# Kernel optimization log

Measured on AMD Instinct MI355X. Metric: run time of the kernel, lower is better.

The kernel has to match this reference:

```python
import jax, jax.numpy as jnp
import numpy as np

HIDDEN = 128
INPUT_SIZE = 64
NUM_ACTIONS = 16
BATCH = 65536


def _uniform(key, shape, scale):
    return jax.random.uniform(key, shape, jnp.float32, -scale, scale)


def setup_inputs() -> dict:
    key = jax.random.key(0)
    ks = jax.random.split(key, 14)
    s = 1.0 / np.sqrt(HIDDEN)  # pytorch LSTM/Linear init scale
    return {
        "x": jax.random.normal(ks[0], (BATCH, INPUT_SIZE), jnp.float32),
        # layer 0 LSTM weights (gate order: i, f, g, o)
        "Wih0": _uniform(ks[1], (4 * HIDDEN, INPUT_SIZE), s),
        "Whh0": _uniform(ks[2], (4 * HIDDEN, HIDDEN), s),
        "bih0": _uniform(ks[3], (4 * HIDDEN,), s),
        "bhh0": _uniform(ks[4], (4 * HIDDEN,), s),
        # layer 1 LSTM weights
        "Wih1": _uniform(ks[5], (4 * HIDDEN, HIDDEN), s),
        "Whh1": _uniform(ks[6], (4 * HIDDEN, HIDDEN), s),
        "bih1": _uniform(ks[7], (4 * HIDDEN,), s),
        "bhh1": _uniform(ks[8], (4 * HIDDEN,), s),
        # policy / value heads
        "Wp": _uniform(ks[9], (NUM_ACTIONS, HIDDEN), s),
        "bp": _uniform(ks[10], (NUM_ACTIONS,), s),
        "Wv": _uniform(ks[11], (1, HIDDEN), s),
        "bv": _uniform(ks[12], (1,), s),
    }


def _lstm_cell(x, h, c, Wih, Whh, bih, bhh):
    # gates: [B, 4H], pytorch gate order i, f, g, o
    g = x @ Wih.T + bih + h @ Whh.T + bhh
    i, f, gg, o = jnp.split(g, 4, axis=-1)
    i = jax.nn.sigmoid(i)
    f = jax.nn.sigmoid(f)
    gg = jnp.tanh(gg)
    o = jax.nn.sigmoid(o)
    c2 = f * c + i * gg
    h2 = o * jnp.tanh(c2)
    return h2, c2


def reference(x, Wih0, Whh0, bih0, bhh0, Wih1, Whh1, bih1, bhh1, Wp, bp, Wv, bv):
    B = x.shape[0]
    z = jnp.zeros((B, HIDDEN), x.dtype)  # state=None -> zero init
    # seq_len == 1: single step through the 2-layer stack
    h0, c0 = _lstm_cell(x, z, z, Wih0, Whh0, bih0, bhh0)
    h1, c1 = _lstm_cell(h0, z, z, Wih1, Whh1, bih1, bhh1)
    out = h1[None]  # [1, B, H] like pytorch LSTM output
    policy = out @ Wp.T + bp  # gumbel=True -> raw logits
    value = out @ Wv.T + bv
    return policy, value
```

## Files before the change

kernel.cpp:

```cpp
#include <hip/hip_runtime.h>
#include <hip/hip_bf16.h>

#define BATCH 65536
#define IN    64
#define H     128
#define NA    16
#define NBLK  256
#define TPB   512

#define NW0   3072
#define NW1   6144
#define NPH   512
#define OW1   3072
#define OPH   9216
#define OBIAS 9728
#define NTOT  9920

typedef __bf16 bf16x8 __attribute__((ext_vector_type(8)));
typedef float  f32x4  __attribute__((ext_vector_type(4)));

union Frag { uint4 u; bf16x8 v; };
struct F32x8 { float4 a, b; };

#define EXP2F(v) __builtin_amdgcn_exp2f(v)
#define RCPF(v)  __builtin_amdgcn_rcpf(v)
#define K1 1.442695041f
#define K2 2.885390082f

__device__ __forceinline__ F32x8 ld8f(const float* p) {
    F32x8 r;
    r.a = *reinterpret_cast<const float4*>(p);
    r.b = *reinterpret_cast<const float4*>(p + 4);
    return r;
}
__device__ __forceinline__ Frag cvt8(F32x8 x) {
    Frag f;
    f.v[0]=(__bf16)x.a.x; f.v[1]=(__bf16)x.a.y; f.v[2]=(__bf16)x.a.z; f.v[3]=(__bf16)x.a.w;
    f.v[4]=(__bf16)x.b.x; f.v[5]=(__bf16)x.b.y; f.v[6]=(__bf16)x.b.z; f.v[7]=(__bf16)x.b.w;
    return f;
}
__device__ __forceinline__ Frag cvt44(float4 a, float4 b) {
    Frag f;
    f.v[0]=(__bf16)a.x; f.v[1]=(__bf16)a.y; f.v[2]=(__bf16)a.z; f.v[3]=(__bf16)a.w;
    f.v[4]=(__bf16)b.x; f.v[5]=(__bf16)b.y; f.v[6]=(__bf16)b.z; f.v[7]=(__bf16)b.w;
    return f;
}
__device__ __forceinline__ unsigned pk2(float lo, float hi) {
    unsigned short l = __builtin_bit_cast(unsigned short, (__bf16)lo);
    unsigned short h = __builtin_bit_cast(unsigned short, (__bf16)hi);
    return (unsigned)l | ((unsigned)h << 16);
}
__device__ __forceinline__ float clamp30(float v) {
    return __builtin_fminf(__builtin_fmaxf(v, -30.0f), 30.0f);
}
__device__ __forceinline__ float lstm_h(float ip, float gp, float op) {
    ip = clamp30(ip); gp = clamp30(gp); op = clamp30(op);
    const float Ei = EXP2F(-K1 * ip);
    const float Eg = EXP2F( K2 * gp);
    const float c2 = (Eg - 1.0f) * RCPF((1.0f + Ei) * (Eg + 1.0f));
    const float Eo = EXP2F(-K1 * op);
    const float Ec = EXP2F( K2 * c2);
    return (Ec - 1.0f) * RCPF((1.0f + Eo) * (Ec + 1.0f));
}

__device__ __forceinline__ int igo_row(int j) {
    const int g = j >> 7, h = j & 127;
    return h + ((g == 0) ? 0 : (g + 1) * 128);
}

__global__ __launch_bounds__(256)
void lstm_prep(const float* __restrict__ Wih0,
               const float* __restrict__ bih0,
               const float* __restrict__ bhh0,
               const float* __restrict__ Wih1,
               const float* __restrict__ bih1,
               const float* __restrict__ bhh1,
               const float* __restrict__ Wp,
               const float* __restrict__ Wv,
               uint4* __restrict__ ws)
{
    const int G = blockIdx.x * 256 + threadIdx.x;
    if (G < NW0) {
        const int j = G >> 3, s = G & 7;
        const int srow = igo_row(j);
        Frag f = cvt8(ld8f(Wih0 + (size_t)srow * IN + s * 8));
        ws[(j << 3) + (s ^ (j & 7))] = f.u;
    } else if (G < OPH) {
        const int t = G - OW1;
        const int j = t >> 4, s = t & 15;
        const int srow = igo_row(j);
        const int kt = s >> 2, qq = s & 3;
        const float* pA = Wih1 + (size_t)srow * H + kt * 32 + qq * 4;
        Frag f = cvt44(*reinterpret_cast<const float4*>(pA),
                       *reinterpret_cast<const float4*>(pA + 16));
        ws[OW1 + (j << 4) + (s ^ (j & 7))] = f.u;
    } else if (G < OBIAS) {
        const int t = G - OPH;
        const int j = t >> 4, s = t & 15;
        const int kt = s >> 2, qq = s & 3;
        Frag f;
        if (j <= 16) {
            const float* base = (j < 16) ? (Wp + (size_t)j * H) : Wv;
            const float* pA = base + kt * 32 + qq * 4;
            f = cvt44(*reinterpret_cast<const float4*>(pA),
                      *reinterpret_cast<const float4*>(pA + 16));
        } else {
            f.u = make_uint4(0u, 0u, 0u, 0u);
        }
        ws[OPH + (j << 4) + (s ^ (j & 7))] = f.u;
    } else if (G < NTOT) {
        const int fbase = (G - OBIAS) * 4;
        float4 r;
#pragma unroll
        for (int e = 0; e < 4; ++e) {
            const int i = fbase + e;
            float v;
            if (i < 384) { const int sr = igo_row(i);        v = bih0[sr] + bhh0[sr]; }
            else         { const int sr = igo_row(i - 384);  v = bih1[sr] + bhh1[sr]; }
            reinterpret_cast<float*>(&r)[e] = v;
        }
        ws[G] = __builtin_bit_cast(uint4, r);
    }
}

__global__ __launch_bounds__(TPB, 2)
void lstm_fused(const float* __restrict__ x,
                const uint4* __restrict__ ws,
                const float* __restrict__ bp,
                const float* __restrict__ bv,
                float* __restrict__ out)
{
    __shared__ __align__(16) uint4 smem[NTOT];

    const int tid  = threadIdx.x;
    const int wave = tid >> 6;
    const int lane = tid & 63;
    const int q    = lane >> 4;
    const int m    = lane & 15;
    const int rbase = blockIdx.x * 256 + wave * 32;
    const f32x4 vzero = {0.f, 0.f, 0.f, 0.f};

    F32x8 xr[2][2];
#pragma unroll
    for (int s2 = 0; s2 < 2; ++s2) {
        const float* xp = x + (size_t)(rbase + s2 * 16 + m) * IN + q * 8;
        xr[s2][0] = ld8f(xp);
        xr[s2][1] = ld8f(xp + 32);
    }
    const float4 bpr = *reinterpret_cast<const float4*>(bp + q * 4);
    const float  bvv = bv[0];

#pragma unroll
    for (int i = tid; i < NTOT; i += TPB) smem[i] = ws[i];

    __syncthreads();

    const uint4* w0s = smem;
    const uint4* w1s = smem + OW1;
    const uint4* wph = smem + OPH;
    const float* b0s = reinterpret_cast<const float*>(smem + OBIAS);
    const float* b1s = b0s + 384;

    const int swz = m & 7;
    Frag xb[2][2];
#pragma unroll
    for (int s2 = 0; s2 < 2; ++s2) {
        xb[s2][0] = cvt8(xr[s2][0]);
        xb[s2][1] = cvt8(xr[s2][1]);
    }

    unsigned hw0[2][16];
#pragma unroll
    for (int nc = 0; nc < 8; ++nc) {
        f32x4 acc[3][2];
#pragma unroll
        for (int g = 0; g < 3; ++g) { acc[g][0] = vzero; acc[g][1] = vzero; }
#pragma unroll
        for (int g = 0; g < 3; ++g) {
            const int n = g * 128 + nc * 16 + m;
#pragma unroll
            for (int kt = 0; kt < 2; ++kt) {
                Frag a; a.u = w0s[(n << 3) + ((kt * 4 + q) ^ swz)];
#pragma unroll
                for (int s2 = 0; s2 < 2; ++s2)
                    acc[g][s2] = __builtin_amdgcn_mfma_f32_16x16x32_bf16(
                        a.v, xb[s2][kt].v, acc[g][s2], 0, 0, 0);
            }
        }
        const f32x4 bI = *reinterpret_cast<const f32x4*>(b0s +       nc * 16 + q * 4);
        const f32x4 bG = *reinterpret_cast<const f32x4*>(b0s + 128 + nc * 16 + q * 4);
        const f32x4 bO = *reinterpret_cast<const f32x4*>(b0s + 256 + nc * 16 + q * 4);
#pragma unroll
        for (int s2 = 0; s2 < 2; ++s2)
#pragma unroll
            for (int u = 0; u < 2; ++u) {
                const float ha = lstm_h(acc[0][s2][2*u]   + bI[2*u],
                                        acc[1][s2][2*u]   + bG[2*u],
                                        acc[2][s2][2*u]   + bO[2*u]);
                const float hb = lstm_h(acc[0][s2][2*u+1] + bI[2*u+1],
                                        acc[1][s2][2*u+1] + bG[2*u+1],
                                        acc[2][s2][2*u+1] + bO[2*u+1]);
                hw0[s2][nc * 2 + u] = pk2(ha, hb);
            }
    }

    unsigned hw1[2][16];
#pragma unroll
    for (int nc = 0; nc < 8; ++nc) {
        f32x4 acc[3][2];
#pragma unroll
        for (int g = 0; g < 3; ++g) { acc[g][0] = vzero; acc[g][1] = vzero; }
#pragma unroll
        for (int kt = 0; kt < 4; ++kt) {
            Frag b[2];
#pragma unroll
            for (int s2 = 0; s2 < 2; ++s2)
                b[s2].u = make_uint4(hw0[s2][4*kt], hw0[s2][4*kt+1],
                                     hw0[s2][4*kt+2], hw0[s2][4*kt+3]);
#pragma unroll
            for (int g = 0; g < 3; ++g) {
                const int n = g * 128 + nc * 16 + m;
                Frag a; a.u = w1s[(n << 4) + ((kt * 4 + q) ^ swz)];
#pragma unroll
                for (int s2 = 0; s2 < 2; ++s2)
                    acc[g][s2] = __builtin_amdgcn_mfma_f32_16x16x32_bf16(
                        a.v, b[s2].v, acc[g][s2], 0, 0, 0);
            }
        }
        const f32x4 bI = *reinterpret_cast<const f32x4*>(b1s +       nc * 16 + q * 4);
        const f32x4 bG = *reinterpret_cast<const f32x4*>(b1s + 128 + nc * 16 + q * 4);
        const f32x4 bO = *reinterpret_cast<const f32x4*>(b1s + 256 + nc * 16 + q * 4);
#pragma unroll
        for (int s2 = 0; s2 < 2; ++s2)
#pragma unroll
            for (int u = 0; u < 2; ++u) {
                const float ha = lstm_h(acc[0][s2][2*u]   + bI[2*u],
                                        acc[1][s2][2*u]   + bG[2*u],
                                        acc[2][s2][2*u]   + bO[2*u]);
                const float hb = lstm_h(acc[0][s2][2*u+1] + bI[2*u+1],
                                        acc[1][s2][2*u+1] + bG[2*u+1],
                                        acc[2][s2][2*u+1] + bO[2*u+1]);
                hw1[s2][nc * 2 + u] = pk2(ha, hb);
            }
    }

    f32x4 ap[2], av[2];
    ap[0] = vzero; ap[1] = vzero; av[0] = vzero; av[1] = vzero;
#pragma unroll
    for (int kt = 0; kt < 4; ++kt) {
        Frag a0; a0.u = wph[( m       << 4) + ((kt * 4 + q) ^ swz)];
        Frag a1; a1.u = wph[((16 + m) << 4) + ((kt * 4 + q) ^ swz)];
#pragma unroll
        for (int s2 = 0; s2 < 2; ++s2) {
            Frag b; b.u = make_uint4(hw1[s2][4*kt], hw1[s2][4*kt+1],
                                     hw1[s2][4*kt+2], hw1[s2][4*kt+3]);
            ap[s2] = __builtin_amdgcn_mfma_f32_16x16x32_bf16(a0.v, b.v, ap[s2], 0, 0, 0);
            av[s2] = __builtin_amdgcn_mfma_f32_16x16x32_bf16(a1.v, b.v, av[s2], 0, 0, 0);
        }
    }
#pragma unroll
    for (int s2 = 0; s2 < 2; ++s2) {
        const int row = rbase + s2 * 16 + m;
        f32x4 po;
        po[0] = ap[s2][0] + bpr.x; po[1] = ap[s2][1] + bpr.y;
        po[2] = ap[s2][2] + bpr.z; po[3] = ap[s2][3] + bpr.w;
        *reinterpret_cast<f32x4*>(out + (size_t)row * NA + q * 4) = po;
        if (q == 0) out[(size_t)BATCH * NA + row] = av[s2][0] + bvv;
    }
}

extern "C" void kernel_launch(void* const* d_in, const int* in_sizes, int n_in,
                              void* d_out, int out_size, void* d_ws, size_t ws_size,
                              hipStream_t stream) {
    uint4* ws = (uint4*)d_ws;
    lstm_prep<<<dim3((NTOT + 255) / 256), dim3(256), 0, stream>>>(
        (const float*)d_in[1], (const float*)d_in[3], (const float*)d_in[4],
        (const float*)d_in[5], (const float*)d_in[7], (const float*)d_in[8],
        (const float*)d_in[9], (const float*)d_in[11], ws);
    lstm_fused<<<dim3(NBLK), dim3(TPB), 0, stream>>>(
        (const float*)d_in[0], ws,
        (const float*)d_in[10], (const float*)d_in[12], (float*)d_out);
}
```

Before: 110.4 us.

## Drop LDS weight staging, read weights from global, widen per-wave batch tile

The fused kernel no longer copies the packed weights into shared memory behind a block barrier. It reads the MFMA A-fragments straight from the global workspace, relying on L1/L2 caching, so the prep kernel's XOR swizzle is removed. Each wave now handles 64 rows instead of 32, with 256 threads per block, so every weight fragment load feeds twice as many MFMAs. Biases are folded into the accumulator initialisation, the clamping is removed, and the gate math is written over float pairs. The risks are global load latency in the inner loop, higher register pressure from four row tiles, and possible overflow in exp2 without the clamp.

```diff
diff --git a/kernel.cpp b/kernel.cpp
--- a/kernel.cpp
+++ b/kernel.cpp
@@ -6,11 +6,8 @@
 #define H     128
 #define NA    16
 #define NBLK  256
-#define TPB   512
-
-#define NW0   3072
-#define NW1   6144
-#define NPH   512
+#define TPB   256
+
 #define OW1   3072
 #define OPH   9216
 #define OBIAS 9728
@@ -18,6 +15,7 @@
 
 typedef __bf16 bf16x8 __attribute__((ext_vector_type(8)));
 typedef float  f32x4  __attribute__((ext_vector_type(4)));
+typedef float  f32x2  __attribute__((ext_vector_type(2)));
 
 union Frag { uint4 u; bf16x8 v; };
 struct F32x8 { float4 a, b; };
@@ -50,17 +48,23 @@
     unsigned short h = __builtin_bit_cast(unsigned short, (__bf16)hi);
     return (unsigned)l | ((unsigned)h << 16);
 }
-__device__ __forceinline__ float clamp30(float v) {
-    return __builtin_fminf(__builtin_fmaxf(v, -30.0f), 30.0f);
-}
-__device__ __forceinline__ float lstm_h(float ip, float gp, float op) {
-    ip = clamp30(ip); gp = clamp30(gp); op = clamp30(op);
-    const float Ei = EXP2F(-K1 * ip);
-    const float Eg = EXP2F( K2 * gp);
-    const float c2 = (Eg - 1.0f) * RCPF((1.0f + Ei) * (Eg + 1.0f));
-    const float Eo = EXP2F(-K1 * op);
-    const float Ec = EXP2F( K2 * c2);
-    return (Ec - 1.0f) * RCPF((1.0f + Eo) * (Ec + 1.0f));
+
+__device__ __forceinline__ unsigned lstm_h2(f32x2 ip, f32x2 gp, f32x2 op) {
+    const f32x2 ai = ip * (-K1);
+    const f32x2 ag = gp * ( K2);
+    f32x2 Ei; Ei[0]=EXP2F(ai[0]); Ei[1]=EXP2F(ai[1]);
+    f32x2 Eg; Eg[0]=EXP2F(ag[0]); Eg[1]=EXP2F(ag[1]);
+    const f32x2 dn = (Ei + 1.0f) * (Eg + 1.0f);
+    f32x2 rd; rd[0]=RCPF(dn[0]); rd[1]=RCPF(dn[1]);
+    const f32x2 c2 = (Eg - 1.0f) * rd;
+    const f32x2 ao = op * (-K1);
+    const f32x2 ac = c2 * ( K2);
+    f32x2 Eo; Eo[0]=EXP2F(ao[0]); Eo[1]=EXP2F(ao[1]);
+    f32x2 Ec; Ec[0]=EXP2F(ac[0]); Ec[1]=EXP2F(ac[1]);
+    const f32x2 dh = (Eo + 1.0f) * (Ec + 1.0f);
+    f32x2 rh; rh[0]=RCPF(dh[0]); rh[1]=RCPF(dh[1]);
+    const f32x2 h = (Ec - 1.0f) * rh;
+    return pk2(h[0], h[1]);
 }
 
 __device__ __forceinline__ int igo_row(int j) {
@@ -80,11 +84,11 @@
                uint4* __restrict__ ws)
 {
     const int G = blockIdx.x * 256 + threadIdx.x;
-    if (G < NW0) {
+    if (G < OW1) {
         const int j = G >> 3, s = G & 7;
         const int srow = igo_row(j);
         Frag f = cvt8(ld8f(Wih0 + (size_t)srow * IN + s * 8));
-        ws[(j << 3) + (s ^ (j & 7))] = f.u;
+        ws[(j << 3) + s] = f.u;
     } else if (G < OPH) {
         const int t = G - OW1;
         const int j = t >> 4, s = t & 15;
@@ -93,7 +97,7 @@
         const float* pA = Wih1 + (size_t)srow * H + kt * 32 + qq * 4;
         Frag f = cvt44(*reinterpret_cast<const float4*>(pA),
                        *reinterpret_cast<const float4*>(pA + 16));
-        ws[OW1 + (j << 4) + (s ^ (j & 7))] = f.u;
+        ws[OW1 + (j << 4) + s] = f.u;
     } else if (G < OBIAS) {
         const int t = G - OPH;
         const int j = t >> 4, s = t & 15;
@@ -107,7 +111,7 @@
         } else {
             f.u = make_uint4(0u, 0u, 0u, 0u);
         }
-        ws[OPH + (j << 4) + (s ^ (j & 7))] = f.u;
+        ws[OPH + (j << 4) + s] = f.u;
     } else if (G < NTOT) {
         const int fbase = (G - OBIAS) * 4;
         float4 r;
@@ -130,142 +134,128 @@
                 const float* __restrict__ bv,
                 float* __restrict__ out)
 {
-    __shared__ __align__(16) uint4 smem[NTOT];
-
     const int tid  = threadIdx.x;
     const int wave = tid >> 6;
     const int lane = tid & 63;
     const int q    = lane >> 4;
     const int m    = lane & 15;
-    const int rbase = blockIdx.x * 256 + wave * 32;
+    const int rbase = blockIdx.x * 256 + wave * 64;
     const f32x4 vzero = {0.f, 0.f, 0.f, 0.f};
 
-    F32x8 xr[2][2];
-#pragma unroll
-    for (int s2 = 0; s2 < 2; ++s2) {
-        const float* xp = x + (size_t)(rbase + s2 * 16 + m) * IN + q * 8;
-        xr[s2][0] = ld8f(xp);
-        xr[s2][1] = ld8f(xp + 32);
+    F32x8 xr[4][2];
+#pragma unroll
+    for (int s4 = 0; s4 < 4; ++s4) {
+        const float* xp = x + (size_t)(rbase + s4 * 16 + m) * IN + q * 8;
+        xr[s4][0] = ld8f(xp);
+        xr[s4][1] = ld8f(xp + 32);
     }
     const float4 bpr = *reinterpret_cast<const float4*>(bp + q * 4);
     const float  bvv = bv[0];
-
-#pragma unroll
-    for (int i = tid; i < NTOT; i += TPB) smem[i] = ws[i];
-
-    __syncthreads();
-
-    const uint4* w0s = smem;
-    const uint4* w1s = smem + OW1;
-    const uint4* wph = smem + OPH;
-    const float* b0s = reinterpret_cast<const float*>(smem + OBIAS);
-    const float* b1s = b0s + 384;
-
-    const int swz = m & 7;
-    Frag xb[2][2];
-#pragma unroll
-    for (int s2 = 0; s2 < 2; ++s2) {
-        xb[s2][0] = cvt8(xr[s2][0]);
-        xb[s2][1] = cvt8(xr[s2][1]);
-    }
-
-    unsigned hw0[2][16];
+    const float* bias = reinterpret_cast<const float*>(ws + OBIAS);
+
+    Frag xb[4][2];
+#pragma unroll
+    for (int s4 = 0; s4 < 4; ++s4) {
+        xb[s4][0] = cvt8(xr[s4][0]);
+        xb[s4][1] = cvt8(xr[s4][1]);
+    }
+
+    unsigned hw0[4][16];
 #pragma unroll
     for (int nc = 0; nc < 8; ++nc) {
-        f32x4 acc[3][2];
-#pragma unroll
-        for (int g = 0; g < 3; ++g) { acc[g][0] = vzero; acc[g][1] = vzero; }
+        const f32x4 bI = *reinterpret_cast<const f32x4*>(bias +       nc * 16 + q * 4);
+        const f32x4 bG = *reinterpret_cast<const f32x4*>(bias + 128 + nc * 16 + q * 4);
+        const f32x4 bO = *reinterpret_cast<const f32x4*>(bias + 256 + nc * 16 + q * 4);
+        f32x4 acc[3][4];
+#pragma unroll
+        for (int s4 = 0; s4 < 4; ++s4) {
+            acc[0][s4] = bI; acc[1][s4] = bG; acc[2][s4] = bO;
+        }
 #pragma unroll
         for (int g = 0; g < 3; ++g) {
             const int n = g * 128 + nc * 16 + m;
 #pragma unroll
             for (int kt = 0; kt < 2; ++kt) {
-                Frag a; a.u = w0s[(n << 3) + ((kt * 4 + q) ^ swz)];
-#pragma unroll
-                for (int s2 = 0; s2 < 2; ++s2)
-                    acc[g][s2] = __builtin_amdgcn_mfma_f32_16x16x32_bf16(
-                        a.v, xb[s2][kt].v, acc[g][s2], 0, 0, 0);
-            }
-        }
-        const f32x4 bI = *reinterpret_cast<const f32x4*>(b0s +       nc * 16 + q * 4);
-        const f32x4 bG = *reinterpret_cast<const f32x4*>(b0s + 128 + nc * 16 + q * 4);
-        const f32x4 bO = *reinterpret_cast<const f32x4*>(b0s + 256 + nc * 16 + q * 4);
-#pragma unroll
-        for (int s2 = 0; s2 < 2; ++s2)
+                Frag a; a.u = ws[(n << 3) + kt * 4 + q];
+#pragma unroll
+                for (int s4 = 0; s4 < 4; ++s4)
+                    acc[g][s4] = __builtin_amdgcn_mfma_f32_16x16x32_bf16(
+                        a.v, xb[s4][kt].v, acc[g][s4], 0, 0, 0);
+            }
+        }
+#pragma unroll
+        for (int s4 = 0; s4 < 4; ++s4)
 #pragma unroll
             for (int u = 0; u < 2; ++u) {
-                const float ha = lstm_h(acc[0][s2][2*u]   + bI[2*u],
-                                        acc[1][s2][2*u]   + bG[2*u],
-                                        acc[2][s2][2*u]   + bO[2*u]);
-                const float hb = lstm_h(acc[0][s2][2*u+1] + bI[2*u+1],
-                                        acc[1][s2][2*u+1] + bG[2*u+1],
-                                        acc[2][s2][2*u+1] + bO[2*u+1]);
-                hw0[s2][nc * 2 + u] = pk2(ha, hb);
-            }
-    }
-
-    unsigned hw1[2][16];
+                const f32x2 ip = {acc[0][s4][2*u], acc[0][s4][2*u+1]};
+                const f32x2 gp = {acc[1][s4][2*u], acc[1][s4][2*u+1]};
+                const f32x2 op = {acc[2][s4][2*u], acc[2][s4][2*u+1]};
+                hw0[s4][nc * 2 + u] = lstm_h2(ip, gp, op);
+            }
+    }
+
+    unsigned hw1[4][16];
 #pragma unroll
     for (int nc = 0; nc < 8; ++nc) {
-        f32x4 acc[3][2];
-#pragma unroll
-        for (int g = 0; g < 3; ++g) { acc[g][0] = vzero; acc[g][1] = vzero; }
+        const f32x4 bI = *reinterpret_cast<const f32x4*>(bias + 384 +       nc * 16 + q * 4);
+        const f32x4 bG = *reinterpret_cast<const f32x4*>(bias + 384 + 128 + nc * 16 + q * 4);
+        const f32x4 bO = *reinterpret_cast<const f32x4*>(bias + 384 + 256 + nc * 16 + q * 4);
+        f32x4 acc[3][4];
+#pragma unroll
+        for (int s4 = 0; s4 < 4; ++s4) {
+            acc[0][s4] = bI; acc[1][s4] = bG; acc[2][s4] = bO;
+        }
 #pragma unroll
         for (int kt = 0; kt < 4; ++kt) {
-            Frag b[2];
-#pragma unroll
-            for (int s2 = 0; s2 < 2; ++s2)
-                b[s2].u = make_uint4(hw0[s2][4*kt], hw0[s2][4*kt+1],
-                                     hw0[s2][4*kt+2], hw0[s2][4*kt+3]);
+            Frag b[4];
+#pragma unroll
+            for (int s4 = 0; s4 < 4; ++s4)
+                b[s4].u = make_uint4(hw0[s4][4*kt], hw0[s4][4*kt+1],
+                                     hw0[s4][4*kt+2], hw0[s4][4*kt+3]);
 #pragma unroll
             for (int g = 0; g < 3; ++g) {
                 const int n = g * 128 + nc * 16 + m;
-                Frag a; a.u = w1s[(n << 4) + ((kt * 4 + q) ^ swz)];
-#pragma unroll
-                for (int s2 = 0; s2 < 2; ++s2)
-                    acc[g][s2] = __builtin_amdgcn_mfma_f32_16x16x32_bf16(
-                        a.v, b[s2].v, acc[g][s2], 0, 0, 0);
-            }
-        }
-        const f32x4 bI = *reinterpret_cast<const f32x4*>(b1s +       nc * 16 + q * 4);
-        const f32x4 bG = *reinterpret_cast<const f32x4*>(b1s + 128 + nc * 16 + q * 4);
-        const f32x4 bO = *reinterpret_cast<const f32x4*>(b1s + 256 + nc * 16 + q * 4);
-#pragma unroll
-        for (int s2 = 0; s2 < 2; ++s2)
+                Frag a; a.u = ws[OW1 + (n << 4) + kt * 4 + q];
+#pragma unroll
+                for (int s4 = 0; s4 < 4; ++s4)
+                    acc[g][s4] = __builtin_amdgcn_mfma_f32_16x16x32_bf16(
+                        a.v, b[s4].v, acc[g][s4], 0, 0, 0);
+            }
+        }
+#pragma unroll
+        for (int s4 = 0; s4 < 4; ++s4)
 #pragma unroll
             for (int u = 0; u < 2; ++u) {
-                const float ha = lstm_h(acc[0][s2][2*u]   + bI[2*u],
-                                        acc[1][s2][2*u]   + bG[2*u],
-                                        acc[2][s2][2*u]   + bO[2*u]);
-                const float hb = lstm_h(acc[0][s2][2*u+1] + bI[2*u+1],
-                                        acc[1][s2][2*u+1] + bG[2*u+1],
-                                        acc[2][s2][2*u+1] + bO[2*u+1]);
-                hw1[s2][nc * 2 + u] = pk2(ha, hb);
-            }
-    }
-
-    f32x4 ap[2], av[2];
-    ap[0] = vzero; ap[1] = vzero; av[0] = vzero; av[1] = vzero;
+                const f32x2 ip = {acc[0][s4][2*u], acc[0][s4][2*u+1]};
+                const f32x2 gp = {acc[1][s4][2*u], acc[1][s4][2*u+1]};
+                const f32x2 op = {acc[2][s4][2*u], acc[2][s4][2*u+1]};
+                hw1[s4][nc * 2 + u] = lstm_h2(ip, gp, op);
+            }
+    }
+
+    f32x4 ap[4], av[4];
+#pragma unroll
+    for (int s4 = 0; s4 < 4; ++s4) { ap[s4] = vzero; av[s4] = vzero; }
 #pragma unroll
     for (int kt = 0; kt < 4; ++kt) {
-        Frag a0; a0.u = wph[( m       << 4) + ((kt * 4 + q) ^ swz)];
-        Frag a1; a1.u = wph[((16 + m) << 4) + ((kt * 4 + q) ^ swz)];
-#pragma unroll
-        for (int s2 = 0; s2 < 2; ++s2) {
-            Frag b; b.u = make_uint4(hw1[s2][4*kt], hw1[s2][4*kt+1],
-                                     hw1[s2][4*kt+2], hw1[s2][4*kt+3]);
-            ap[s2] = __builtin_amdgcn_mfma_f32_16x16x32_bf16(a0.v, b.v, ap[s2], 0, 0, 0);
-            av[s2] = __builtin_amdgcn_mfma_f32_16x16x32_bf16(a1.v, b.v, av[s2], 0, 0, 0);
-        }
-    }
-#pragma unroll
-    for (int s2 = 0; s2 < 2; ++s2) {
-        const int row = rbase + s2 * 16 + m;
+        Frag a0; a0.u = ws[OPH + ( m       << 4) + kt * 4 + q];
+        Frag a1; a1.u = ws[OPH + ((16 + m) << 4) + kt * 4 + q];
+#pragma unroll
+        for (int s4 = 0; s4 < 4; ++s4) {
+            Frag b; b.u = make_uint4(hw1[s4][4*kt], hw1[s4][4*kt+1],
+                                     hw1[s4][4*kt+2], hw1[s4][4*kt+3]);
+            ap[s4] = __builtin_amdgcn_mfma_f32_16x16x32_bf16(a0.v, b.v, ap[s4], 0, 0, 0);
+            av[s4] = __builtin_amdgcn_mfma_f32_16x16x32_bf16(a1.v, b.v, av[s4], 0, 0, 0);
+        }
+    }
+#pragma unroll
+    for (int s4 = 0; s4 < 4; ++s4) {
+        const int row = rbase + s4 * 16 + m;
         f32x4 po;
-        po[0] = ap[s2][0] + bpr.x; po[1] = ap[s2][1] + bpr.y;
-        po[2] = ap[s2][2] + bpr.z; po[3] = ap[s2][3] + bpr.w;
+        po[0] = ap[s4][0] + bpr.x; po[1] = ap[s4][1] + bpr.y;
+        po[2] = ap[s4][2] + bpr.z; po[3] = ap[s4][3] + bpr.w;
         *reinterpret_cast<f32x4*>(out + (size_t)row * NA + q * 4) = po;
-        if (q == 0) out[(size_t)BATCH * NA + row] = av[s2][0] + bvv;
+        if (q == 0) out[(size_t)BATCH * NA + row] = av[s4][0] + bvv;
     }
 }
 
```

Measured after the change: 110.2 us. Within noise of the previous version (-0.2%).
